# Performance work log

Measured on AMD Instinct MI355X. Metric: run time of the kernel, lower is better.

## Reference

```python
import jax, jax.numpy as jnp
import numpy as np

V, E, H = 348, 512, 1024  # vocab, embed dim, GRU hidden


def gru_cell(x, h, w_ih, w_hh, b_ih, b_hh):
    # PyTorch GRUCell: gates ordered [r, z, n] along the 3H axis
    gi = x @ w_ih.T + b_ih            # [B, 3H]
    gh = h @ w_hh.T + b_hh            # [B, 3H]
    i_r, i_z, i_n = jnp.split(gi, 3, axis=-1)
    h_r, h_z, h_n = jnp.split(gh, 3, axis=-1)
    r = jax.nn.sigmoid(i_r + h_r)
    z = jax.nn.sigmoid(i_z + h_z)
    n = jnp.tanh(i_n + r * h_n)
    return (1.0 - z) * n + z * h


def setup_inputs() -> dict:
    key = jax.random.key(0)
    ks = jax.random.split(key, 20)
    B, T = 256, 128
    p = lambda k, shape: jax.random.normal(k, shape, dtype=jnp.float32) * 0.02
    return {
        "target": jax.random.randint(ks[0], (B, T), 0, V, dtype=jnp.int32),
        "bos": 1,
        "emb": p(ks[1], (V, E)),
        "w_ih1": p(ks[2], (3 * H, E)),  "w_hh1": p(ks[3], (3 * H, H)),
        "b_ih1": p(ks[4], (3 * H,)),    "b_hh1": p(ks[5], (3 * H,)),
        "w_ih2": p(ks[6], (3 * H, H)),  "w_hh2": p(ks[7], (3 * H, H)),
        "b_ih2": p(ks[8], (3 * H,)),    "b_hh2": p(ks[9], (3 * H,)),
        "w_ih3": p(ks[10], (3 * H, H)), "w_hh3": p(ks[11], (3 * H, H)),
        "b_ih3": p(ks[12], (3 * H,)),   "b_hh3": p(ks[13], (3 * H,)),
        "w_out": p(ks[14], (V, H)),     "b_out": p(ks[15], (V,)),
    }


def reference(target, bos, emb, w_ih1, w_hh1, b_ih1, b_hh1,
              w_ih2, w_hh2, b_ih2, b_hh2,
              w_ih3, w_hh3, b_ih3, b_hh3, w_out, b_out):
    B, T = target.shape
    # input tokens = [<bos>, target[:, :-1]]
    x_in = jnp.concatenate(
        [jnp.full((B, 1), bos, dtype=target.dtype), target[:, :-1]], axis=1)
    h0 = jnp.zeros((B, H), jnp.float32)
    lp0 = jnp.zeros((B,), jnp.float32)

    def step(carry, xt):
        h1, h2, h3, lp = carry
        tok, tgt = xt                     # [B], [B]
        e = emb[tok]                      # [B, E]
        h1 = gru_cell(e, h1, w_ih1, w_hh1, b_ih1, b_hh1)
        h2 = gru_cell(h1, h2, w_ih2, w_hh2, b_ih2, b_hh2)
        h3 = gru_cell(h2, h3, w_ih3, w_hh3, b_ih3, b_hh3)
        logits = h3 @ w_out.T + b_out     # [B, V]
        logp = jax.nn.log_softmax(logits, axis=-1)
        # NLLLoss in source = sum(one_hot(tgt) * log_prob) = gathered log-prob
        lp = lp + jnp.take_along_axis(logp, tgt[:, None], axis=1)[:, 0]
        return (h1, h2, h3, lp), None

    (_, _, _, log_probs), _ = jax.lax.scan(
        step, (h0, h0, h0, lp0), (x_in.T, target.T))
    return log_probs
```

## Files before the change

### kernel.cpp

```cpp
#include <hip/hip_runtime.h>
#include <hip/hip_bf16.h>
#include <cstdint>

constexpr int kT = 128;
constexpr int kB = 256;
constexpr int kE = 512;
constexpr int kH = 1024;
constexpr int kV = 348;
constexpr int kNG = 3072;
constexpr int NB = 208;

constexpr float kScale = 32.f;
constexpr float kInvSS = 1.f / 1024.f;

typedef float f4v __attribute__((ext_vector_type(4)));
typedef unsigned short u16;
typedef unsigned char u8;

__device__ __forceinline__ u8 f2e4m3(float x) {
  int p = __builtin_amdgcn_cvt_pk_fp8_f32(x, x, 0, false);
  return (u8)(p & 0xff);
}

__device__ __forceinline__ uint64_t ldv_u64(const void* p) {
  return __hip_atomic_load((const uint64_t*)p, __ATOMIC_RELAXED, __HIP_MEMORY_SCOPE_AGENT);
}
__device__ __forceinline__ void stv_u8(u8* p, u8 v) {
  __hip_atomic_store(p, v, __ATOMIC_RELAXED, __HIP_MEMORY_SCOPE_AGENT);
}

__device__ __forceinline__ int permn(int n) {
  int gate = n >> 10, j = n & 1023;
  return ((j >> 4) * 48) + gate * 16 + (j & 15);
}

struct Params {
  const int* target; const int* bosp; const float* b_out;
  const u8 *w1i, *w1h, *w2i, *w2h, *w3i, *w3h, *wout, *embb;
  const float *bi1, *bh1, *bi2, *bh2, *bi3, *bh3;
  float *h1f, *h2f, *h3f;
  u8    *h1b, *h2b, *h3b;
  float *lp;
  unsigned *acnt; unsigned *gflag;
};

union SMem {
  struct { u8 A[128 * 128]; u8 B[96 * 128]; } mm;
  float logits[16 * 400];
};

#define BAR_LDS() asm volatile("s_waitcnt lgkmcnt(0)\n\ts_barrier" ::: "memory")

__device__ __forceinline__ void gbar(unsigned* acnt, unsigned* gflag, unsigned s) {
  asm volatile("s_waitcnt vmcnt(0)" ::: "memory");
  __syncthreads();
  if (threadIdx.x == 0) {
    const unsigned g = blockIdx.x & 31u;
    __hip_atomic_fetch_add(&acnt[g * 16], 1u, __ATOMIC_RELAXED, __HIP_MEMORY_SCOPE_AGENT);
    if (blockIdx.x == 0) {
      for (;;) {
        unsigned sum = 0;
#pragma unroll
        for (int i = 0; i < 32; ++i)
          sum += __hip_atomic_load(&acnt[i * 16], __ATOMIC_RELAXED, __HIP_MEMORY_SCOPE_AGENT);
        if (sum >= (unsigned)NB * (s + 1u)) break;
        __builtin_amdgcn_s_sleep(4);
      }
#pragma unroll
      for (int i = 0; i < 32; ++i)
        __hip_atomic_store(&gflag[i * 16], s + 1u, __ATOMIC_RELAXED, __HIP_MEMORY_SCOPE_AGENT);
    } else {
      while (__hip_atomic_load(&gflag[g * 16], __ATOMIC_RELAXED, __HIP_MEMORY_SCOPE_AGENT) <= s)
        __builtin_amdgcn_s_sleep(8);
    }
    asm volatile("" ::: "memory");
  }
  __syncthreads();
}

#define LOAD_A(dst, k0)                                                      \
  _Pragma("unroll")                                                          \
  for (int p = 0; p < 4; ++p) {                                              \
    int id = p * 256 + t, r = id >> 3, c = id & 7;                           \
    if (EMB) {                                                               \
      int tok = (u == 0) ? bos : target[(b0 + r) * kT + (u - 1)];            \
      uint4 v = *(const uint4*)&Asrc[(size_t)tok * K + (k0) + c * 16];       \
      dst[p][0] = ((uint64_t)v.y << 32) | v.x;                               \
      dst[p][1] = ((uint64_t)v.w << 32) | v.z;                               \
    } else {                                                                 \
      const u8* srcp = Asrc + (size_t)(b0 + r) * kH + (k0) + c * 16;         \
      dst[p][0] = ldv_u64(srcp); dst[p][1] = ldv_u64(srcp + 8);              \
    }                                                                        \
  }

#define LOAD_B(dst, k0)                                                      \
  _Pragma("unroll")                                                          \
  for (int p = 0; p < 3; ++p) {                                              \
    int id = p * 256 + t, r = id >> 3, c = id & 7;                           \
    dst[p] = *(const uint4*)&W[(size_t)(n0 + r) * K + (k0) + c * 16];        \
  }

#define WR_AB(srcA, srcB)                                                    \
  _Pragma("unroll")                                                          \
  for (int p = 0; p < 4; ++p) {                                              \
    int id = p * 256 + t, r = id >> 3, c = id & 7;                           \
    const int u0 = c * 2, rx = r & 15;                                       \
    u8* base = &sm.mm.A[r * 128];                                            \
    *(uint64_t*)(base + 8 * (u0 ^ rx)) = srcA[p][0];                         \
    *(uint64_t*)(base + 8 * ((u0 + 1) ^ rx)) = srcA[p][1];                   \
  }                                                                          \
  _Pragma("unroll")                                                          \
  for (int p = 0; p < 3; ++p) {                                              \
    int id = p * 256 + t, r = id >> 3, c = id & 7;                           \
    const int u0 = c * 2, rx = r & 15;                                       \
    u8* base = &sm.mm.B[r * 128];                                            \
    *(uint64_t*)(base + 8 * (u0 ^ rx)) = (uint64_t)srcB[p].x | ((uint64_t)srcB[p].y << 32); \
    *(uint64_t*)(base + 8 * ((u0 + 1) ^ rx)) = (uint64_t)srcB[p].z | ((uint64_t)srcB[p].w << 32); \
  }

#define MFMA_TILE()                                                          \
  _Pragma("unroll")                                                          \
  for (int kk = 0; kk < 128; kk += 32) {                                     \
    const int swz = 8 * (((kk >> 3) + q) ^ li);                              \
    long a[4], bb[3];                                                        \
    _Pragma("unroll")                                                        \
    for (int m2 = 0; m2 < 4; ++m2)                                           \
      a[m2] = *(const long*)&sm.mm.A[(64 * wm + 16 * m2 + li) * 128 + swz];  \
    _Pragma("unroll")                                                        \
    for (int g = 0; g < 3; ++g)                                              \
      bb[g] = *(const long*)&sm.mm.B[(48 * wg + 16 * g + li) * 128 + swz];   \
    _Pragma("unroll")                                                        \
    for (int m2 = 0; m2 < 4; ++m2) {                                         \
      aR[m2] = __builtin_amdgcn_mfma_f32_16x16x32_fp8_fp8(a[m2], bb[0], aR[m2], 0, 0, 0); \
      aZ[m2] = __builtin_amdgcn_mfma_f32_16x16x32_fp8_fp8(a[m2], bb[1], aZ[m2], 0, 0, 0); \
      aN[m2] = __builtin_amdgcn_mfma_f32_16x16x32_fp8_fp8(a[m2], bb[2], aN[m2], 0, 0, 0); \
    }                                                                        \
  }

template<int K, bool EMB>
__device__ __forceinline__ void mm_phase(SMem& sm, const u8* __restrict__ Asrc,
    const u8* __restrict__ W, int b0, int n0,
    f4v* aR, f4v* aZ, f4v* aN,
    const int* __restrict__ target, int bos, int u)
{
  const int t = threadIdx.x, lane = t & 63, wv = t >> 6;
  const int wm = wv >> 1, wg = wv & 1, li = lane & 15, q = lane >> 4;
  constexpr int NT = K / 128;
  uint64_t raE[4][2], raO[4][2];
  uint4 rbE[3], rbO[3];

  LOAD_A(raE, 0)
  LOAD_B(rbE, 0)
  LOAD_A(raO, 128)
  LOAD_B(rbO, 128)

#pragma unroll 1
  for (int it = 0; it < NT; it += 2) {
    BAR_LDS();
    WR_AB(raE, rbE)
    BAR_LDS();
    if (it + 2 < NT) { LOAD_A(raE, (it + 2) * 128) LOAD_B(rbE, (it + 2) * 128) }
    MFMA_TILE()
    BAR_LDS();
    WR_AB(raO, rbO)
    BAR_LDS();
    if (it + 3 < NT) { LOAD_A(raO, (it + 3) * 128) LOAD_B(rbO, (it + 3) * 128) }
    MFMA_TILE()
  }
}

template<int K1, bool L1>
__device__ void do_L(SMem& sm, const u8* __restrict__ xsrc,
                     const u8* __restrict__ hbPrev, const float* __restrict__ hfPrev,
                     const u8* __restrict__ Wih, const u8* __restrict__ Whh,
                     const float* __restrict__ biP, const float* __restrict__ bhP,
                     float* __restrict__ hfOut, u8* __restrict__ hbOut,
                     const int* __restrict__ target, int bos, int u, int mt, int jt)
{
  const int b0 = mt * 128, j0 = jt * 32, n0 = jt * 96;
  f4v aR[4], aZ[4], aNi[4], aNh[4];
#pragma unroll
  for (int i = 0; i < 4; ++i) {
    aR[i] = f4v{0.f,0.f,0.f,0.f}; aZ[i] = f4v{0.f,0.f,0.f,0.f};
    aNi[i] = f4v{0.f,0.f,0.f,0.f}; aNh[i] = f4v{0.f,0.f,0.f,0.f};
  }
  mm_phase<K1, L1>(sm, xsrc, Wih, b0, n0, aR, aZ, aNi, target, bos, u);
  mm_phase<kH, false>(sm, hbPrev, Whh, b0, n0, aR, aZ, aNh, target, bos, u);

  const int t = threadIdx.x, lane = t & 63, wv = t >> 6;
  const int wm = wv >> 1, wg = wv & 1, li = lane & 15, q = lane >> 4;
  const int j = j0 + 16 * wg + li;
  const int cr = n0 + 48 * wg + li;
  const float bR = biP[cr] + bhP[cr];
  const float bZ = biP[cr + 16] + bhP[cr + 16];
  const float biN = biP[cr + 32], bhN = bhP[cr + 32];
  float hold[4][4];
#pragma unroll
  for (int m2 = 0; m2 < 4; ++m2)
#pragma unroll
    for (int r = 0; r < 4; ++r) {
      int b = b0 + 64 * wm + 16 * m2 + 4 * q + r;
      hold[m2][r] = hfPrev[(size_t)b * kH + j];
    }
#pragma unroll
  for (int m2 = 0; m2 < 4; ++m2)
#pragma unroll
    for (int r = 0; r < 4; ++r) {
      int b = b0 + 64 * wm + 16 * m2 + 4 * q + r;
      float rg = 1.f / (1.f + __expf(-(aR[m2][r] * kInvSS + bR)));
      float zg = 1.f / (1.f + __expf(-(aZ[m2][r] * kInvSS + bZ)));
      float np = (aNi[m2][r] * kInvSS + biN) + rg * (aNh[m2][r] * kInvSS + bhN);
      float nh = 2.f / (1.f + __expf(-2.f * np)) - 1.f;
      float hnew = (1.f - zg) * nh + zg * hold[m2][r];
      hfOut[(size_t)b * kH + j] = hnew;
      stv_u8(&hbOut[(size_t)b * kH + j], f2e4m3(hnew * kScale));
    }
}

__device__ void do_E(SMem& sm, const u8* __restrict__ h3b, const u8* __restrict__ wo,
                     const float* __restrict__ b_out, const int* __restrict__ target,
                     float* __restrict__ lp, int u, int tile)
{
  const int b0 = tile * 16;
  const int t = threadIdx.x, lane = t & 63, wv = t >> 6;
  const int li = lane & 15, q = lane >> 4;

  {
    const int row = t & 15, th = t >> 4;
    const int q2 = th & 3, kc = th >> 2;
    const u8* srcb = h3b + (size_t)(b0 + row) * kH + q2 * 8;
    uint64_t s0 = ldv_u64(srcb + (0 * 4 + kc) * 32);
    uint64_t s1 = ldv_u64(srcb + (1 * 4 + kc) * 32);
    uint64_t s2 = ldv_u64(srcb + (2 * 4 + kc) * 32);
    uint64_t s3 = ldv_u64(srcb + (3 * 4 + kc) * 32);
    uint64_t s4 = ldv_u64(srcb + (4 * 4 + kc) * 32);
    uint64_t s5 = ldv_u64(srcb + (5 * 4 + kc) * 32);
    uint64_t s6 = ldv_u64(srcb + (6 * 4 + kc) * 32);
    uint64_t s7 = ldv_u64(srcb + (7 * 4 + kc) * 32);
    u8* db = &sm.mm.A[kc * 512 + row * 32 + q2 * 8];
    *(uint64_t*)(db + 0 * 2048) = s0;
    *(uint64_t*)(db + 1 * 2048) = s1;
    *(uint64_t*)(db + 2 * 2048) = s2;
    *(uint64_t*)(db + 3 * 2048) = s3;
    *(uint64_t*)(db + 4 * 2048) = s4;
    *(uint64_t*)(db + 5 * 2048) = s5;
    *(uint64_t*)(db + 6 * 2048) = s6;
    *(uint64_t*)(db + 7 * 2048) = s7;
  }
  __syncthreads();

  f4v acc[6];
#pragma unroll
  for (int f = 0; f < 6; ++f) acc[f] = f4v{0.f, 0.f, 0.f, 0.f};

  const u8* wp = wo + (size_t)(96 * wv + li) * kH + q * 8;
  const u8* al = &sm.mm.A[li * 32 + q * 8];

  uint64_t bE[6], bO[6];
#pragma unroll
  for (int f = 0; f < 6; ++f) bE[f] = *(const uint64_t*)(wp + (size_t)16 * f * kH);
#pragma unroll
  for (int f = 0; f < 6; ++f) bO[f] = *(const uint64_t*)(wp + (size_t)16 * f * kH + 32);

#pragma unroll 1
  for (int k0 = 0; k0 < kH; k0 += 64) {
    uint64_t bT[6];
    if (k0 + 64 < kH) {
#pragma unroll
      for (int f = 0; f < 6; ++f) bT[f] = *(const uint64_t*)(wp + (size_t)16 * f * kH + k0 + 64);
    }
    const uint64_t aE = *(const uint64_t*)(al + (k0 >> 5) * 512);
#pragma unroll
    for (int f = 0; f < 6; ++f)
      acc[f] = __builtin_amdgcn_mfma_f32_16x16x32_fp8_fp8((long)aE, (long)bE[f], acc[f], 0, 0, 0);
    if (k0 + 64 < kH) {
#pragma unroll
      for (int f = 0; f < 6; ++f) bE[f] = bT[f];
    }
    if (k0 + 96 < kH) {
#pragma unroll
      for (int f = 0; f < 6; ++f) bT[f] = *(const uint64_t*)(wp + (size_t)16 * f * kH + k0 + 96);
    }
    const uint64_t aO = *(const uint64_t*)(al + ((k0 + 32) >> 5) * 512);
#pragma unroll
    for (int f = 0; f < 6; ++f)
      acc[f] = __builtin_amdgcn_mfma_f32_16x16x32_fp8_fp8((long)aO, (long)bO[f], acc[f], 0, 0, 0);
    if (k0 + 96 < kH) {
#pragma unroll
      for (int f = 0; f < 6; ++f) bO[f] = bT[f];
    }
  }
  __syncthreads();
#pragma unroll
  for (int f = 0; f < 6; ++f) {
    int n = 96 * wv + 16 * f + li;
    if (n < kV) {
      float bo = b_out[n];
#pragma unroll
      for (int r = 0; r < 4; ++r)
        sm.logits[(4 * q + r) * 400 + n] = acc[f][r] * kInvSS + bo;
    }
  }
  __syncthreads();
  int m = 4 * wv + q;
  int b = b0 + m;
  float mx = -1e30f;
  for (int cc = li; cc < kV; cc += 16) mx = fmaxf(mx, sm.logits[m * 400 + cc]);
#pragma unroll
  for (int d = 1; d < 16; d <<= 1) mx = fmaxf(mx, __shfl_xor(mx, d, 16));
  float se = 0.f;
  for (int cc = li; cc < kV; cc += 16) se += __expf(sm.logits[m * 400 + cc] - mx);
#pragma unroll
  for (int d = 1; d < 16; d <<= 1) se += __shfl_xor(se, d, 16);
  int tgt = target[b * kT + u];
  float logp = sm.logits[m * 400 + tgt] - mx - __logf(se);
  if (li == 0) lp[b] += logp;
}

__global__ __launch_bounds__(256, 1) void rnn_main(Params P)
{
  __shared__ SMem sm;
  const int bid = blockIdx.x;
  const int bos = P.bosp[0];
  const size_t HS = (size_t)kB * kH;

  const int local = bid & 63;
  const int mt = (local >> 3) & 1;
  const int jt = (local & 7) | ((local >> 4) << 3);

  for (int s = 0; s < kT + 3; ++s) {
    if (bid < 64) {
      int u = s;
      if (u < kT)
        do_L<kE, true>(sm, P.embb,
                       P.h1b + (size_t)((u - 1) & 1) * HS, P.h1f + (size_t)((u - 1) & 1) * HS,
                       P.w1i, P.w1h, P.bi1, P.bh1,
                       P.h1f + (size_t)(u & 1) * HS, P.h1b + (size_t)(u & 1) * HS,
                       P.target, bos, u, mt, jt);
    } else if (bid < 128) {
      int u = s - 1;
      if (u >= 0 && u < kT)
        do_L<kH, false>(sm, P.h1b + (size_t)(u & 1) * HS,
                        P.h2b + (size_t)((u - 1) & 1) * HS, P.h2f + (size_t)((u - 1) & 1) * HS,
                        P.w2i, P.w2h, P.bi2, P.bh2,
                        P.h2f + (size_t)(u & 1) * HS, P.h2b + (size_t)(u & 1) * HS,
                        P.target, bos, u, mt, jt);
    } else if (bid < 192) {
      int u = s - 2;
      if (u >= 0 && u < kT)
        do_L<kH, false>(sm, P.h2b + (size_t)(u & 1) * HS,
                        P.h3b + (size_t)((u - 1) & 1) * HS, P.h3f + (size_t)((u - 1) & 1) * HS,
                        P.w3i, P.w3h, P.bi3, P.bh3,
                        P.h3f + (size_t)(u & 1) * HS, P.h3b + (size_t)(u & 1) * HS,
                        P.target, bos, u, mt, jt);
    } else {
      int u = s - 3;
      if (u >= 0 && u < kT)
        do_E(sm, P.h3b + (size_t)(u & 1) * HS, P.wout, P.b_out, P.target, P.lp, u, bid - 192);
    }
    gbar(P.acnt, P.gflag, (unsigned)s);
  }
}

__global__ void k_conv_w(const float* __restrict__ w, u8* __restrict__ wp, int K, int logK) {
  int idx = blockIdx.x * 256 + threadIdx.x;
  if (idx >= kNG * K) return;
  int n = idx >> logK, k = idx & (K - 1);
  wp[(size_t)permn(n) * K + k] = f2e4m3(w[idx] * kScale);
}
__global__ void k_conv_b(const float* __restrict__ b, float* __restrict__ bp) {
  int idx = blockIdx.x * 256 + threadIdx.x;
  if (idx < kNG) bp[permn(idx)] = b[idx];
}
__global__ void k_conv_wout(const float* __restrict__ w, u8* __restrict__ wp) {
  int idx = blockIdx.x * 256 + threadIdx.x;
  if (idx >= 384 * kH) return;
  int n = idx >> 10, k = idx & 1023;
  wp[idx] = (n < kV) ? f2e4m3(w[(size_t)n * kH + k] * kScale) : (u8)0;
}
__global__ void k_conv_emb(const float* __restrict__ e, u8* __restrict__ ep) {
  int idx = blockIdx.x * 256 + threadIdx.x;
  if (idx < kV * kE) ep[idx] = f2e4m3(e[idx] * kScale);
}

extern "C" void kernel_launch(void* const* d_in, const int* in_sizes, int n_in,
                              void* d_out, int out_size, void* d_ws, size_t ws_size,
                              hipStream_t stream)
{
  const int*   target = (const int*)d_in[0];
  const int*   bosp   = (const int*)d_in[1];
  const float* emb    = (const float*)d_in[2];
  const float* w_ih1  = (const float*)d_in[3];
  const float* w_hh1  = (const float*)d_in[4];
  const float* b_ih1  = (const float*)d_in[5];
  const float* b_hh1  = (const float*)d_in[6];
  const float* w_ih2  = (const float*)d_in[7];
  const float* w_hh2  = (const float*)d_in[8];
  const float* b_ih2  = (const float*)d_in[9];
  const float* b_hh2  = (const float*)d_in[10];
  const float* w_ih3  = (const float*)d_in[11];
  const float* w_hh3  = (const float*)d_in[12];
  const float* b_ih3  = (const float*)d_in[13];
  const float* b_hh3  = (const float*)d_in[14];
  const float* w_out  = (const float*)d_in[15];
  const float* b_out  = (const float*)d_in[16];

  char* ws = (char*)d_ws;
  size_t off = 0;
  auto alloc = [&](size_t bytes) -> void* {
    void* p = ws + off;
    off = (off + bytes + 511) & ~(size_t)511;
    return p;
  };
  u8* w1i = (u8*)alloc((size_t)kNG * kE);
  u8* w1h = (u8*)alloc((size_t)kNG * kH);
  u8* w2i = (u8*)alloc((size_t)kNG * kH);
  u8* w2h = (u8*)alloc((size_t)kNG * kH);
  u8* w3i = (u8*)alloc((size_t)kNG * kH);
  u8* w3h = (u8*)alloc((size_t)kNG * kH);
  u8* wo  = (u8*)alloc((size_t)384 * kH);
  u8* eb  = (u8*)alloc((size_t)kV * kE);
  float* bi1 = (float*)alloc(kNG * 4);
  float* bh1 = (float*)alloc(kNG * 4);
  float* bi2 = (float*)alloc(kNG * 4);
  float* bh2 = (float*)alloc(kNG * 4);
  float* bi3 = (float*)alloc(kNG * 4);
  float* bh3 = (float*)alloc(kNG * 4);
  float* h1f = (float*)alloc((size_t)2 * kB * kH * 4);
  float* h2f = (float*)alloc((size_t)2 * kB * kH * 4);
  float* h3f = (float*)alloc((size_t)2 * kB * kH * 4);
  u8* h1b = (u8*)alloc((size_t)2 * kB * kH);
  u8* h2b = (u8*)alloc((size_t)2 * kB * kH);
  u8* h3b = (u8*)alloc((size_t)2 * kB * kH);
  unsigned* bar = (unsigned*)alloc(4096);
  (void)ws_size; (void)in_sizes; (void)n_in; (void)out_size;

  k_conv_w<<<(kNG * kE + 255) / 256, 256, 0, stream>>>(w_ih1, w1i, kE, 9);
  k_conv_w<<<(kNG * kH + 255) / 256, 256, 0, stream>>>(w_hh1, w1h, kH, 10);
  k_conv_w<<<(kNG * kH + 255) / 256, 256, 0, stream>>>(w_ih2, w2i, kH, 10);
  k_conv_w<<<(kNG * kH + 255) / 256, 256, 0, stream>>>(w_hh2, w2h, kH, 10);
  k_conv_w<<<(kNG * kH + 255) / 256, 256, 0, stream>>>(w_ih3, w3i, kH, 10);
  k_conv_w<<<(kNG * kH + 255) / 256, 256, 0, stream>>>(w_hh3, w3h, kH, 10);
  k_conv_b<<<(kNG + 255) / 256, 256, 0, stream>>>(b_ih1, bi1);
  k_conv_b<<<(kNG + 255) / 256, 256, 0, stream>>>(b_hh1, bh1);
  k_conv_b<<<(kNG + 255) / 256, 256, 0, stream>>>(b_ih2, bi2);
  k_conv_b<<<(kNG + 255) / 256, 256, 0, stream>>>(b_hh2, bh2);
  k_conv_b<<<(kNG + 255) / 256, 256, 0, stream>>>(b_ih3, bi3);
  k_conv_b<<<(kNG + 255) / 256, 256, 0, stream>>>(b_hh3, bh3);
  k_conv_wout<<<(384 * kH + 255) / 256, 256, 0, stream>>>(w_out, wo);
  k_conv_emb<<<(kV * kE + 255) / 256, 256, 0, stream>>>(emb, eb);

  hipMemsetAsync(h1f, 0, (size_t)3 * 2 * kB * kH * 4, stream);
  hipMemsetAsync(h1b, 0, (size_t)3 * 2 * kB * kH, stream);
  hipMemsetAsync(bar, 0, 4096, stream);
  hipMemsetAsync(d_out, 0, (size_t)kB * 4, stream);

  Params P;
  P.target = target; P.bosp = bosp; P.b_out = b_out;
  P.w1i = w1i; P.w1h = w1h; P.w2i = w2i; P.w2h = w2h; P.w3i = w3i; P.w3h = w3h;
  P.wout = wo; P.embb = eb;
  P.bi1 = bi1; P.bh1 = bh1; P.bi2 = bi2; P.bh2 = bh2; P.bi3 = bi3; P.bh3 = bh3;
  P.h1f = h1f; P.h2f = h2f; P.h3f = h3f;
  P.h1b = h1b; P.h2b = h2b; P.h3b = h3b;
  P.lp = (float*)d_out;
  P.acnt = bar; P.gflag = bar + 512;

  rnn_main<<<dim3(NB), dim3(256), 0, stream>>>(P);
}
```

Measured before the change: 3.764 ms.

## Replace global per-step barrier with per-layer dataflow counters

Drops the grid-wide barrier that ran after every pipeline step and replaces it with per-layer, per-batch-half counters. Each block waits only on the producer, its own layer's previous step, and the consumer's progress (so the double buffer can be reused safely). This lets layers run ahead of each other and removes the cost of all 208 blocks joining a central barrier. It adds more atomic polling points and relies on relaxed atomics for ordering, which may be fragile.

```diff
diff --git a/kernel.cpp b/kernel.cpp
--- a/kernel.cpp
+++ b/kernel.cpp
@@ -51,31 +51,19 @@
 
 #define BAR_LDS() asm volatile("s_waitcnt lgkmcnt(0)\n\ts_barrier" ::: "memory")
 
-__device__ __forceinline__ void gbar(unsigned* acnt, unsigned* gflag, unsigned s) {
+__device__ __forceinline__ void wait_ge(unsigned* c, unsigned tgt) {
+  if (threadIdx.x == 0) {
+    while (__hip_atomic_load(c, __ATOMIC_RELAXED, __HIP_MEMORY_SCOPE_AGENT) < tgt)
+      __builtin_amdgcn_s_sleep(4);
+    asm volatile("" ::: "memory");
+  }
+  __syncthreads();
+}
+__device__ __forceinline__ void signal_cnt(unsigned* c) {
   asm volatile("s_waitcnt vmcnt(0)" ::: "memory");
   __syncthreads();
-  if (threadIdx.x == 0) {
-    const unsigned g = blockIdx.x & 31u;
-    __hip_atomic_fetch_add(&acnt[g * 16], 1u, __ATOMIC_RELAXED, __HIP_MEMORY_SCOPE_AGENT);
-    if (blockIdx.x == 0) {
-      for (;;) {
-        unsigned sum = 0;
-#pragma unroll
-        for (int i = 0; i < 32; ++i)
-          sum += __hip_atomic_load(&acnt[i * 16], __ATOMIC_RELAXED, __HIP_MEMORY_SCOPE_AGENT);
-        if (sum >= (unsigned)NB * (s + 1u)) break;
-        __builtin_amdgcn_s_sleep(4);
-      }
-#pragma unroll
-      for (int i = 0; i < 32; ++i)
-        __hip_atomic_store(&gflag[i * 16], s + 1u, __ATOMIC_RELAXED, __HIP_MEMORY_SCOPE_AGENT);
-    } else {
-      while (__hip_atomic_load(&gflag[g * 16], __ATOMIC_RELAXED, __HIP_MEMORY_SCOPE_AGENT) <= s)
-        __builtin_amdgcn_s_sleep(8);
-    }
-    asm volatile("" ::: "memory");
-  }
-  __syncthreads();
+  if (threadIdx.x == 0)
+    __hip_atomic_fetch_add(c, 1u, __ATOMIC_RELAXED, __HIP_MEMORY_SCOPE_AGENT);
 }
 
 #define LOAD_A(dst, k0)                                                      \
@@ -169,13 +157,14 @@
   }
 }
 
-template<int K1, bool L1>
+template<int K1, bool L1f>
 __device__ void do_L(SMem& sm, const u8* __restrict__ xsrc,
                      const u8* __restrict__ hbPrev, const float* __restrict__ hfPrev,
                      const u8* __restrict__ Wih, const u8* __restrict__ Whh,
                      const float* __restrict__ biP, const float* __restrict__ bhP,
                      float* __restrict__ hfOut, u8* __restrict__ hbOut,
-                     const int* __restrict__ target, int bos, int u, int mt, int jt)
+                     const int* __restrict__ target, int bos, int u, int mt, int jt,
+                     unsigned* prodP, unsigned* selfP, unsigned* consP, unsigned consMul)
 {
   const int b0 = mt * 128, j0 = jt * 32, n0 = jt * 96;
   f4v aR[4], aZ[4], aNi[4], aNh[4];
@@ -184,7 +173,9 @@
     aR[i] = f4v{0.f,0.f,0.f,0.f}; aZ[i] = f4v{0.f,0.f,0.f,0.f};
     aNi[i] = f4v{0.f,0.f,0.f,0.f}; aNh[i] = f4v{0.f,0.f,0.f,0.f};
   }
-  mm_phase<K1, L1>(sm, xsrc, Wih, b0, n0, aR, aZ, aNi, target, bos, u);
+  if (!L1f) wait_ge(prodP, 32u * (unsigned)(u + 1));
+  mm_phase<K1, L1f>(sm, xsrc, Wih, b0, n0, aR, aZ, aNi, target, bos, u);
+  if (u >= 1) wait_ge(selfP, 32u * (unsigned)u);
   mm_phase<kH, false>(sm, hbPrev, Whh, b0, n0, aR, aZ, aNh, target, bos, u);
 
   const int t = threadIdx.x, lane = t & 63, wv = t >> 6;
@@ -202,6 +193,7 @@
       int b = b0 + 64 * wm + 16 * m2 + 4 * q + r;
       hold[m2][r] = hfPrev[(size_t)b * kH + j];
     }
+  if (u >= 2) wait_ge(consP, consMul * (unsigned)(u - 1));
 #pragma unroll
   for (int m2 = 0; m2 < 4; ++m2)
 #pragma unroll
@@ -215,16 +207,19 @@
       hfOut[(size_t)b * kH + j] = hnew;
       stv_u8(&hbOut[(size_t)b * kH + j], f2e4m3(hnew * kScale));
     }
+  signal_cnt(selfP);
 }
 
 __device__ void do_E(SMem& sm, const u8* __restrict__ h3b, const u8* __restrict__ wo,
                      const float* __restrict__ b_out, const int* __restrict__ target,
-                     float* __restrict__ lp, int u, int tile)
+                     float* __restrict__ lp, int u, int tile,
+                     unsigned* prodP, unsigned* selfP)
 {
   const int b0 = tile * 16;
   const int t = threadIdx.x, lane = t & 63, wv = t >> 6;
   const int li = lane & 15, q = lane >> 4;
 
+  wait_ge(prodP, 32u * (unsigned)(u + 1));
   {
     const int row = t & 15, th = t >> 4;
     const int q2 = th & 3, kc = th >> 2;
@@ -248,6 +243,8 @@
     *(uint64_t*)(db + 7 * 2048) = s7;
   }
   __syncthreads();
+  if (threadIdx.x == 0)
+    __hip_atomic_fetch_add(selfP, 1u, __ATOMIC_RELAXED, __HIP_MEMORY_SCOPE_AGENT);
 
   f4v acc[6];
 #pragma unroll
@@ -315,6 +312,7 @@
   int tgt = target[b * kT + u];
   float logp = sm.logits[m * 400 + tgt] - mx - __logf(se);
   if (li == 0) lp[b] += logp;
+  __syncthreads();
 }
 
 __global__ __launch_bounds__(256, 1) void rnn_main(Params P)
@@ -324,41 +322,47 @@
   const int bos = P.bosp[0];
   const size_t HS = (size_t)kB * kH;
 
-  const int local = bid & 63;
-  const int mt = (local >> 3) & 1;
-  const int jt = (local & 7) | ((local >> 4) << 3);
-
-  for (int s = 0; s < kT + 3; ++s) {
+  unsigned* C = P.acnt;
+  #define P1c(m) (C + 0   + (m) * 16)
+  #define P2c(m) (C + 64  + (m) * 16)
+  #define P3c(m) (C + 128 + (m) * 16)
+  #define PEc(m) (C + 192 + (m) * 16)
+
+  if (bid < 192) {
+    const int local = bid & 63;
+    const int mt = (local >> 3) & 1;
+    const int jt = (local & 7) | ((local >> 4) << 3);
     if (bid < 64) {
-      int u = s;
-      if (u < kT)
+      for (int u = 0; u < kT; ++u)
         do_L<kE, true>(sm, P.embb,
                        P.h1b + (size_t)((u - 1) & 1) * HS, P.h1f + (size_t)((u - 1) & 1) * HS,
                        P.w1i, P.w1h, P.bi1, P.bh1,
                        P.h1f + (size_t)(u & 1) * HS, P.h1b + (size_t)(u & 1) * HS,
-                       P.target, bos, u, mt, jt);
+                       P.target, bos, u, mt, jt,
+                       nullptr, P1c(mt), P2c(mt), 32u);
     } else if (bid < 128) {
-      int u = s - 1;
-      if (u >= 0 && u < kT)
+      for (int u = 0; u < kT; ++u)
         do_L<kH, false>(sm, P.h1b + (size_t)(u & 1) * HS,
                         P.h2b + (size_t)((u - 1) & 1) * HS, P.h2f + (size_t)((u - 1) & 1) * HS,
                         P.w2i, P.w2h, P.bi2, P.bh2,
                         P.h2f + (size_t)(u & 1) * HS, P.h2b + (size_t)(u & 1) * HS,
-                        P.target, bos, u, mt, jt);
-    } else if (bid < 192) {
-      int u = s - 2;
-      if (u >= 0 && u < kT)
+                        P.target, bos, u, mt, jt,
+                        P1c(mt), P2c(mt), P3c(mt), 32u);
+    } else {
+      for (int u = 0; u < kT; ++u)
         do_L<kH, false>(sm, P.h2b + (size_t)(u & 1) * HS,
                         P.h3b + (size_t)((u - 1) & 1) * HS, P.h3f + (size_t)((u - 1) & 1) * HS,
                         P.w3i, P.w3h, P.bi3, P.bh3,
                         P.h3f + (size_t)(u & 1) * HS, P.h3b + (size_t)(u & 1) * HS,
-                        P.target, bos, u, mt, jt);
-    } else {
-      int u = s - 3;
-      if (u >= 0 && u < kT)
-        do_E(sm, P.h3b + (size_t)(u & 1) * HS, P.wout, P.b_out, P.target, P.lp, u, bid - 192);
-    }
-    gbar(P.acnt, P.gflag, (unsigned)s);
+                        P.target, bos, u, mt, jt,
+                        P2c(mt), P3c(mt), PEc(mt), 8u);
+    }
+  } else {
+    const int tile = bid - 192;
+    const int mt = tile >> 3;
+    for (int u = 0; u < kT; ++u)
+      do_E(sm, P.h3b + (size_t)(u & 1) * HS, P.wout, P.b_out, P.target, P.lp, u, tile,
+           P3c(mt), PEc(mt));
   }
 }
 
```

Measured after the change: 3.892 ms. 1.03x slower.

## Cover the full batch per block with 512 threads and halve the grid

Applied to the files above, without the earlier changes.

Each GRU-layer block now computes all 256 batch rows for its 96 gate columns, using 8 waves and a 256x128 A tile in LDS. Previously two blocks each handled 128 rows and both loaded the same weight tile. The output-projection blocks now handle 32 rows each. The grid drops from 208 to 104 blocks, which halves weight traffic per step and the number of grid-barrier participants. In exchange, each step's matmul work sits on half as many CUs, so per-block latency on the recurrent critical path roughly doubles.

```diff
diff --git a/kernel.cpp b/kernel.cpp
--- a/kernel.cpp
+++ b/kernel.cpp
@@ -8,7 +8,7 @@
 constexpr int kH = 1024;
 constexpr int kV = 348;
 constexpr int kNG = 3072;
-constexpr int NB = 208;
+constexpr int NB = 104;
 
 constexpr float kScale = 32.f;
 constexpr float kInvSS = 1.f / 1024.f;
@@ -45,8 +45,8 @@
 };
 
 union SMem {
-  struct { u8 A[128 * 128]; u8 B[96 * 128]; } mm;
-  float logits[16 * 400];
+  struct { u8 A[256 * 128]; u8 B[96 * 128]; } mm;
+  float logits[32 * 400];
 };
 
 #define BAR_LDS() asm volatile("s_waitcnt lgkmcnt(0)\n\ts_barrier" ::: "memory")
@@ -81,41 +81,47 @@
 #define LOAD_A(dst, k0)                                                      \
   _Pragma("unroll")                                                          \
   for (int p = 0; p < 4; ++p) {                                              \
-    int id = p * 256 + t, r = id >> 3, c = id & 7;                           \
+    int id = p * 512 + t, r = id >> 3, c = id & 7;                           \
     if (EMB) {                                                               \
-      int tok = (u == 0) ? bos : target[(b0 + r) * kT + (u - 1)];            \
+      int tok = (u == 0) ? bos : target[r * kT + (u - 1)];                   \
       uint4 v = *(const uint4*)&Asrc[(size_t)tok * K + (k0) + c * 16];       \
       dst[p][0] = ((uint64_t)v.y << 32) | v.x;                               \
       dst[p][1] = ((uint64_t)v.w << 32) | v.z;                               \
     } else {                                                                 \
-      const u8* srcp = Asrc + (size_t)(b0 + r) * kH + (k0) + c * 16;         \
+      const u8* srcp = Asrc + (size_t)r * kH + (k0) + c * 16;                \
       dst[p][0] = ldv_u64(srcp); dst[p][1] = ldv_u64(srcp + 8);              \
     }                                                                        \
   }
 
 #define LOAD_B(dst, k0)                                                      \
   _Pragma("unroll")                                                          \
-  for (int p = 0; p < 3; ++p) {                                              \
-    int id = p * 256 + t, r = id >> 3, c = id & 7;                           \
-    dst[p] = *(const uint4*)&W[(size_t)(n0 + r) * K + (k0) + c * 16];        \
+  for (int p = 0; p < 2; ++p) {                                              \
+    int id = p * 512 + t;                                                    \
+    if (id < 768) {                                                          \
+      int r = id >> 3, c = id & 7;                                           \
+      dst[p] = *(const uint4*)&W[(size_t)(n0 + r) * K + (k0) + c * 16];      \
+    }                                                                        \
   }
 
 #define WR_AB(srcA, srcB)                                                    \
   _Pragma("unroll")                                                          \
   for (int p = 0; p < 4; ++p) {                                              \
-    int id = p * 256 + t, r = id >> 3, c = id & 7;                           \
+    int id = p * 512 + t, r = id >> 3, c = id & 7;                           \
     const int u0 = c * 2, rx = r & 15;                                       \
     u8* base = &sm.mm.A[r * 128];                                            \
     *(uint64_t*)(base + 8 * (u0 ^ rx)) = srcA[p][0];                         \
     *(uint64_t*)(base + 8 * ((u0 + 1) ^ rx)) = srcA[p][1];                   \
   }                                                                          \
   _Pragma("unroll")                                                          \
-  for (int p = 0; p < 3; ++p) {                                              \
-    int id = p * 256 + t, r = id >> 3, c = id & 7;                           \
-    const int u0 = c * 2, rx = r & 15;                                       \
-    u8* base = &sm.mm.B[r * 128];                                            \
-    *(uint64_t*)(base + 8 * (u0 ^ rx)) = (uint64_t)srcB[p].x | ((uint64_t)srcB[p].y << 32); \
-    *(uint64_t*)(base + 8 * ((u0 + 1) ^ rx)) = (uint64_t)srcB[p].z | ((uint64_t)srcB[p].w << 32); \
+  for (int p = 0; p < 2; ++p) {                                              \
+    int id = p * 512 + t;                                                    \
+    if (id < 768) {                                                          \
+      int r = id >> 3, c = id & 7;                                           \
+      const int u0 = c * 2, rx = r & 15;                                     \
+      u8* base = &sm.mm.B[r * 128];                                          \
+      *(uint64_t*)(base + 8 * (u0 ^ rx)) = (uint64_t)srcB[p].x | ((uint64_t)srcB[p].y << 32); \
+      *(uint64_t*)(base + 8 * ((u0 + 1) ^ rx)) = (uint64_t)srcB[p].z | ((uint64_t)srcB[p].w << 32); \
+    }                                                                        \
   }
 
 #define MFMA_TILE()                                                          \
@@ -139,7 +145,7 @@
 
 template<int K, bool EMB>
 __device__ __forceinline__ void mm_phase(SMem& sm, const u8* __restrict__ Asrc,
-    const u8* __restrict__ W, int b0, int n0,
+    const u8* __restrict__ W, int n0,
     f4v* aR, f4v* aZ, f4v* aN,
     const int* __restrict__ target, int bos, int u)
 {
@@ -147,7 +153,7 @@
   const int wm = wv >> 1, wg = wv & 1, li = lane & 15, q = lane >> 4;
   constexpr int NT = K / 128;
   uint64_t raE[4][2], raO[4][2];
-  uint4 rbE[3], rbO[3];
+  uint4 rbE[2], rbO[2];
 
   LOAD_A(raE, 0)
   LOAD_B(rbE, 0)
@@ -169,23 +175,23 @@
   }
 }
 
-template<int K1, bool L1>
+template<int K1, bool L1f>
 __device__ void do_L(SMem& sm, const u8* __restrict__ xsrc,
                      const u8* __restrict__ hbPrev, const float* __restrict__ hfPrev,
                      const u8* __restrict__ Wih, const u8* __restrict__ Whh,
                      const float* __restrict__ biP, const float* __restrict__ bhP,
                      float* __restrict__ hfOut, u8* __restrict__ hbOut,
-                     const int* __restrict__ target, int bos, int u, int mt, int jt)
+                     const int* __restrict__ target, int bos, int u, int jt)
 {
-  const int b0 = mt * 128, j0 = jt * 32, n0 = jt * 96;
+  const int j0 = jt * 32, n0 = jt * 96;
   f4v aR[4], aZ[4], aNi[4], aNh[4];
 #pragma unroll
   for (int i = 0; i < 4; ++i) {
     aR[i] = f4v{0.f,0.f,0.f,0.f}; aZ[i] = f4v{0.f,0.f,0.f,0.f};
     aNi[i] = f4v{0.f,0.f,0.f,0.f}; aNh[i] = f4v{0.f,0.f,0.f,0.f};
   }
-  mm_phase<K1, L1>(sm, xsrc, Wih, b0, n0, aR, aZ, aNi, target, bos, u);
-  mm_phase<kH, false>(sm, hbPrev, Whh, b0, n0, aR, aZ, aNh, target, bos, u);
+  mm_phase<K1, L1f>(sm, xsrc, Wih, n0, aR, aZ, aNi, target, bos, u);
+  mm_phase<kH, false>(sm, hbPrev, Whh, n0, aR, aZ, aNh, target, bos, u);
 
   const int t = threadIdx.x, lane = t & 63, wv = t >> 6;
   const int wm = wv >> 1, wg = wv & 1, li = lane & 15, q = lane >> 4;
@@ -199,14 +205,14 @@
   for (int m2 = 0; m2 < 4; ++m2)
 #pragma unroll
     for (int r = 0; r < 4; ++r) {
-      int b = b0 + 64 * wm + 16 * m2 + 4 * q + r;
+      int b = 64 * wm + 16 * m2 + 4 * q + r;
       hold[m2][r] = hfPrev[(size_t)b * kH + j];
     }
 #pragma unroll
   for (int m2 = 0; m2 < 4; ++m2)
 #pragma unroll
     for (int r = 0; r < 4; ++r) {
-      int b = b0 + 64 * wm + 16 * m2 + 4 * q + r;
+      int b = 64 * wm + 16 * m2 + 4 * q + r;
       float rg = 1.f / (1.f + __expf(-(aR[m2][r] * kInvSS + bR)));
       float zg = 1.f / (1.f + __expf(-(aZ[m2][r] * kInvSS + bZ)));
       float np = (aNi[m2][r] * kInvSS + biN) + rg * (aNh[m2][r] * kInvSS + bhN);
@@ -219,16 +225,18 @@
 
 __device__ void do_E(SMem& sm, const u8* __restrict__ h3b, const u8* __restrict__ wo,
                      const float* __restrict__ b_out, const int* __restrict__ target,
-                     float* __restrict__ lp, int u, int tile)
+                     float* __restrict__ lp, int u, int pairIdx)
 {
-  const int b0 = tile * 16;
+  const int b0 = pairIdx * 32;
   const int t = threadIdx.x, lane = t & 63, wv = t >> 6;
   const int li = lane & 15, q = lane >> 4;
+  const int half = wv >> 2, wq = wv & 3;
 
   {
-    const int row = t & 15, th = t >> 4;
+    const int hh = t >> 8, tt = t & 255;
+    const int row = tt & 15, th = tt >> 4;
     const int q2 = th & 3, kc = th >> 2;
-    const u8* srcb = h3b + (size_t)(b0 + row) * kH + q2 * 8;
+    const u8* srcb = h3b + (size_t)(b0 + hh * 16 + row) * kH + q2 * 8;
     uint64_t s0 = ldv_u64(srcb + (0 * 4 + kc) * 32);
     uint64_t s1 = ldv_u64(srcb + (1 * 4 + kc) * 32);
     uint64_t s2 = ldv_u64(srcb + (2 * 4 + kc) * 32);
@@ -237,7 +245,7 @@
     uint64_t s5 = ldv_u64(srcb + (5 * 4 + kc) * 32);
     uint64_t s6 = ldv_u64(srcb + (6 * 4 + kc) * 32);
     uint64_t s7 = ldv_u64(srcb + (7 * 4 + kc) * 32);
-    u8* db = &sm.mm.A[kc * 512 + row * 32 + q2 * 8];
+    u8* db = &sm.mm.A[hh * 16384 + kc * 512 + row * 32 + q2 * 8];
     *(uint64_t*)(db + 0 * 2048) = s0;
     *(uint64_t*)(db + 1 * 2048) = s1;
     *(uint64_t*)(db + 2 * 2048) = s2;
@@ -253,8 +261,8 @@
 #pragma unroll
   for (int f = 0; f < 6; ++f) acc[f] = f4v{0.f, 0.f, 0.f, 0.f};
 
-  const u8* wp = wo + (size_t)(96 * wv + li) * kH + q * 8;
-  const u8* al = &sm.mm.A[li * 32 + q * 8];
+  const u8* wp = wo + (size_t)(96 * wq + li) * kH + q * 8;
+  const u8* al = &sm.mm.A[half * 16384 + li * 32 + q * 8];
 
   uint64_t bE[6], bO[6];
 #pragma unroll
@@ -293,16 +301,16 @@
   __syncthreads();
 #pragma unroll
   for (int f = 0; f < 6; ++f) {
-    int n = 96 * wv + 16 * f + li;
+    int n = 96 * wq + 16 * f + li;
     if (n < kV) {
       float bo = b_out[n];
 #pragma unroll
       for (int r = 0; r < 4; ++r)
-        sm.logits[(4 * q + r) * 400 + n] = acc[f][r] * kInvSS + bo;
-    }
-  }
-  __syncthreads();
-  int m = 4 * wv + q;
+        sm.logits[(half * 16 + 4 * q + r) * 400 + n] = acc[f][r] * kInvSS + bo;
+    }
+  }
+  __syncthreads();
+  int m = half * 16 + 4 * wq + q;
   int b = b0 + m;
   float mx = -1e30f;
   for (int cc = li; cc < kV; cc += 16) mx = fmaxf(mx, sm.logits[m * 400 + cc]);
@@ -315,48 +323,46 @@
   int tgt = target[b * kT + u];
   float logp = sm.logits[m * 400 + tgt] - mx - __logf(se);
   if (li == 0) lp[b] += logp;
-}
-
-__global__ __launch_bounds__(256, 1) void rnn_main(Params P)
+  __syncthreads();
+}
+
+__global__ __launch_bounds__(512, 1) void rnn_main(Params P)
 {
   __shared__ SMem sm;
   const int bid = blockIdx.x;
   const int bos = P.bosp[0];
   const size_t HS = (size_t)kB * kH;
-
-  const int local = bid & 63;
-  const int mt = (local >> 3) & 1;
-  const int jt = (local & 7) | ((local >> 4) << 3);
+  const int jt = bid & 31;
 
   for (int s = 0; s < kT + 3; ++s) {
-    if (bid < 64) {
+    if (bid < 32) {
       int u = s;
       if (u < kT)
         do_L<kE, true>(sm, P.embb,
                        P.h1b + (size_t)((u - 1) & 1) * HS, P.h1f + (size_t)((u - 1) & 1) * HS,
                        P.w1i, P.w1h, P.bi1, P.bh1,
                        P.h1f + (size_t)(u & 1) * HS, P.h1b + (size_t)(u & 1) * HS,
-                       P.target, bos, u, mt, jt);
-    } else if (bid < 128) {
+                       P.target, bos, u, jt);
+    } else if (bid < 64) {
       int u = s - 1;
       if (u >= 0 && u < kT)
         do_L<kH, false>(sm, P.h1b + (size_t)(u & 1) * HS,
                         P.h2b + (size_t)((u - 1) & 1) * HS, P.h2f + (size_t)((u - 1) & 1) * HS,
                         P.w2i, P.w2h, P.bi2, P.bh2,
                         P.h2f + (size_t)(u & 1) * HS, P.h2b + (size_t)(u & 1) * HS,
-                        P.target, bos, u, mt, jt);
-    } else if (bid < 192) {
+                        P.target, bos, u, jt);
+    } else if (bid < 96) {
       int u = s - 2;
       if (u >= 0 && u < kT)
         do_L<kH, false>(sm, P.h2b + (size_t)(u & 1) * HS,
                         P.h3b + (size_t)((u - 1) & 1) * HS, P.h3f + (size_t)((u - 1) & 1) * HS,
                         P.w3i, P.w3h, P.bi3, P.bh3,
                         P.h3f + (size_t)(u & 1) * HS, P.h3b + (size_t)(u & 1) * HS,
-                        P.target, bos, u, mt, jt);
+                        P.target, bos, u, jt);
     } else {
       int u = s - 3;
       if (u >= 0 && u < kT)
-        do_E(sm, P.h3b + (size_t)(u & 1) * HS, P.wout, P.b_out, P.target, P.lp, u, bid - 192);
+        do_E(sm, P.h3b + (size_t)(u & 1) * HS, P.wout, P.b_out, P.target, P.lp, u, bid - 96);
     }
     gbar(P.acnt, P.gflag, (unsigned)s);
   }
@@ -465,5 +471,5 @@
   P.lp = (float*)d_out;
   P.acnt = bar; P.gflag = bar + 512;
 
-  rnn_main<<<dim3(NB), dim3(256), 0, stream>>>(P);
-}
+  rnn_main<<<dim3(NB), dim3(512), 0, stream>>>(P);
+}
```

After: 6.915 ms. +83.7%, slower.
